# Optimization experiments

Measured on AMD Instinct MI355X. Metric: run time of the kernel, lower is better.

The kernel has to match this reference:

```python
import jax, jax.numpy as jnp
import numpy as np
import math
from functools import lru_cache

N_NODES = 30000
N_EDGES = 360000
IN_CH = 256
EDGE_DIM = 64

def parse_irreps(s):
    out = []
    for t in s.split('+'):
        t = t.strip()
        mul, lp = t.split('x')
        out.append((int(mul), int(lp[:-1]), 1 if lp[-1] == 'e' else -1))
    return out

IRR0 = parse_irreps('16x0e')
IRR1 = parse_irreps('16x0e + 2x1o + 2x2e')
IRR2 = parse_irreps('16x0e + 2x1o + 2x1e + 2x2e + 2x2o')
IRR3 = parse_irreps('2x0e + 2x0o + 2x1e + 2x1o + 2x2e + 2x2o + 2x3e + 2x3o')
SH_IRR = parse_irreps('1x0e + 1x1o + 1x2e')

def irreps_dim(irr):
    return sum(m * (2 * l + 1) for m, l, _ in irr)

def instructions(in1, in2, out):
    ins = []
    for i1, (m1, l1, p1) in enumerate(in1):
        for i2, (m2, l2, p2) in enumerate(in2):
            for io, (m3, l3, p3) in enumerate(out):
                if p1 * p2 == p3 and abs(l1 - l2) <= l3 <= l1 + l2:
                    ins.append((i1, i2, io, m1, m2, m3, l1, l2, l3))
    return ins

def weight_numel(in1, in2, out):
    return sum(t[3] * t[4] * t[5] for t in instructions(in1, in2, out))

def _su2_cg(j1, m1, j2, m2, j3, m3):
    if m3 != m1 + m2:
        return 0.0
    f = math.factorial
    vmin = max(-j1 + j2 + m3, -j1 + m1, 0)
    vmax = min(j2 + j3 + m1, j3 - j1 + j2, j3 + m3)
    if vmax < vmin:
        return 0.0
    c = math.sqrt((2 * j3 + 1) * f(j3 + j1 - j2) * f(j3 - j1 + j2) * f(j1 + j2 - j3) * f(j3 + m3) * f(j3 - m3) / (f(j1 + j2 + j3 + 1) * f(j1 - m1) * f(j1 + m1) * f(j2 - m2) * f(j2 + m2)))
    s = 0.0
    for v in range(vmin, vmax + 1):
        s += (-1.0) ** (v + j2 + m2) * f(j2 + j3 + m1 - v) * f(j1 - m1 + v) / (f(v) * f(j3 - j1 + j2 - v) * f(j3 + m3 - v) * f(v + j1 - j2 - m3))
    return c * s

def _q(l):
    q = np.zeros((2 * l + 1, 2 * l + 1), dtype=np.complex128)
    for m in range(-l, 0):
        q[l + m, l + abs(m)] = 2 ** -0.5
        q[l + m, l - abs(m)] = -1j * 2 ** -0.5
    q[l, l] = 1.0
    for m in range(1, l + 1):
        q[l + m, l + abs(m)] = (-1) ** m * 2 ** -0.5
        q[l + m, l - abs(m)] = 1j * (-1) ** m * 2 ** -0.5
    return (-1j) ** l * q

@lru_cache(maxsize=None)
def wigner_3j(l1, l2, l3):
    cg = np.zeros((2 * l1 + 1, 2 * l2 + 1, 2 * l3 + 1), dtype=np.complex128)
    for m1 in range(-l1, l1 + 1):
        for m2 in range(-l2, l2 + 1):
            for m3 in range(-l3, l3 + 1):
                cg[l1 + m1, l2 + m2, l3 + m3] = _su2_cg(l1, m1, l2, m2, l3, m3)
    c = np.einsum('ij,kl,nm,ikn->jlm', _q(l1), _q(l2), np.conj(_q(l3)), cg)
    cr, ci = np.real(c), np.imag(c)
    c = cr if np.linalg.norm(cr) >= np.linalg.norm(ci) else ci
    return jnp.asarray(c / np.linalg.norm(c), dtype=jnp.float32)

def slices(irr):
    offs, o = [], 0
    for m, l, _ in irr:
        offs.append(o)
        o += m * (2 * l + 1)
    return offs

def tensor_product(in1, in2, out, x1, x2, w):
    # e3nn FullyConnectedTensorProduct with external (per-edge) weights
    s1, s2, so = slices(in1), slices(in2), slices(out)
    ins = instructions(in1, in2, out)
    fan = {}
    for _, _, io, m1, m2, _, _, _, _ in ins:
        fan[io] = fan.get(io, 0) + m1 * m2
    e = x1.shape[0]
    res = jnp.zeros((e, irreps_dim(out)), x1.dtype)
    wo = 0
    for i1, i2, io, m1, m2, m3, l1, l2, l3 in ins:
        a = x1[:, s1[i1]:s1[i1] + m1 * (2 * l1 + 1)].reshape(e, m1, 2 * l1 + 1)
        b = x2[:, s2[i2]:s2[i2] + m2 * (2 * l2 + 1)].reshape(e, m2, 2 * l2 + 1)
        nw = m1 * m2 * m3
        ww = w[:, wo:wo + nw].reshape(e, m1, m2, m3)
        wo += nw
        c3 = wigner_3j(l1, l2, l3)
        alpha = math.sqrt((2 * l3 + 1) / fan[io])
        r = alpha * jnp.einsum('ijk,euvw,eui,evj->ewk', c3, ww, a, b)
        res = res.at[:, so[io]:so[io] + m3 * (2 * l3 + 1)].add(r.reshape(e, m3 * (2 * l3 + 1)))
    return res

def sph_harm(vec):
    # '1x0e + 1x1o + 1x2e', normalize=True, 'component' normalization
    n = jnp.sqrt(jnp.sum(vec * vec, axis=-1, keepdims=True))
    u = vec / jnp.maximum(n, 1e-12)
    x, y, z = u[..., 0], u[..., 1], u[..., 2]
    s3, s5, s15 = math.sqrt(3.0), math.sqrt(5.0), math.sqrt(15.0)
    return jnp.stack([jnp.ones_like(x), s3 * y, s3 * z, s3 * x, s15 * x * y, s15 * y * z, 0.5 * s5 * (3 * z * z - 1.0), s15 * x * z, 0.5 * s15 * (x * x - y * y)], axis=-1)

def conv_layer(in_irr, out_irr, node, edge_index, edge_feat, edge_sh, w1, b1, w2, b2, residual):
    src, dst = edge_index[0], edge_index[1]
    w = jax.nn.softplus(edge_feat @ w1 + b1) @ w2 + b2
    tp = tensor_product(in_irr, SH_IRR, out_irr, node[dst], edge_sh, w)
    n = node.shape[0]
    tot = jax.ops.segment_sum(tp, src, num_segments=n)
    cnt = jax.ops.segment_sum(jnp.ones((tp.shape[0],), tp.dtype), src, num_segments=n)
    out = tot / jnp.maximum(cnt, 1.0)[:, None]
    if residual:
        out = out + jnp.pad(node, ((0, 0), (0, out.shape[-1] - node.shape[-1])))
    return out

def _forward(node_feature, edge_vec, edge_feature, edge_index, lin_w, lin_b, f1w1, f1b1, f1w2, f1b2, f2w1, f2b1, f2w2, f2b2, f3w1, f3b1, f3w2, f3b2):
    edge_sh = sph_harm(edge_vec)
    h = node_feature @ lin_w + lin_b
    h = conv_layer(IRR0, IRR1, h, edge_index, edge_feature, edge_sh, f1w1, f1b1, f1w2, f1b2, True)
    h = conv_layer(IRR1, IRR2, h, edge_index, edge_feature, edge_sh, f2w1, f2b1, f2w2, f2b2, False)
    h = conv_layer(IRR2, IRR3, h, edge_index, edge_feature, edge_sh, f3w1, f3b1, f3w2, f3b2, False)
    return h

def setup_inputs() -> dict:
    key = jax.random.key(0)
    ks = jax.random.split(key, 20)
    def rn(k, shape, scale=1.0):
        return scale * jax.random.normal(k, shape, dtype=jnp.float32)
    inp = dict(
        node_feature=rn(ks[0], (N_NODES, IN_CH)),
        edge_vec=rn(ks[1], (N_EDGES, 3)),
        edge_feature=rn(ks[2], (N_EDGES, EDGE_DIM)),
        edge_index=jax.random.randint(ks[3], (2, N_EDGES), 0, N_NODES, dtype=jnp.int32),
        lin_w=rn(ks[4], (IN_CH, 16), IN_CH ** -0.5),
        lin_b=jnp.zeros((16,), jnp.float32),
    )
    wns = [weight_numel(IRR0, SH_IRR, IRR1), weight_numel(IRR1, SH_IRR, IRR2), weight_numel(IRR2, SH_IRR, IRR3)]
    for i, wn in enumerate(wns, 1):
        inp['fc%d_w1' % i] = rn(ks[4 + 4 * i], (EDGE_DIM, EDGE_DIM), EDGE_DIM ** -0.5)
        inp['fc%d_b1' % i] = jnp.zeros((EDGE_DIM,), jnp.float32)
        inp['fc%d_w2' % i] = rn(ks[5 + 4 * i], (EDGE_DIM, wn), EDGE_DIM ** -0.5)
        inp['fc%d_b2' % i] = jnp.zeros((wn,), jnp.float32)
    return inp

def reference(node_feature, edge_vec, edge_feature, edge_index, lin_w, lin_b, fc1_w1, fc1_b1, fc1_w2, fc1_b2, fc2_w1, fc2_b1, fc2_w2, fc2_b2, fc3_w1, fc3_b1, fc3_w2, fc3_b2):
    return _forward(node_feature, edge_vec, edge_feature, edge_index, lin_w, lin_b, fc1_w1, fc1_b1, fc1_w2, fc1_b2, fc2_w1, fc2_b1, fc2_w2, fc2_b2, fc3_w1, fc3_b1, fc3_w2, fc3_b2)
```

## Files before the change

### kernel.cpp

```cpp
#include <hip/hip_runtime.h>
#include <math.h>

#define EDGES 360000
#define NODES 30000
#define NB_SCAN 118
#define EPB 48

typedef _Float16 h2 __attribute__((ext_vector_type(2)));
typedef _Float16 h8 __attribute__((ext_vector_type(8)));

__device__ inline int imin(int a, int b){ return a < b ? a : b; }
__device__ inline int imax(int a, int b){ return a > b ? a : b; }

__device__ __forceinline__ float fdot2h(h2 a, h2 b, float c){
#if __has_builtin(__builtin_amdgcn_fdot2)
  return __builtin_amdgcn_fdot2(a, b, c, false);
#else
  return c + (float)a[0]*(float)b[0] + (float)a[1]*(float)b[1];
#endif
}

__device__ __forceinline__ float softplusf(float v){
  return fmaxf(v, 0.f) + log1pf(expf(-fabsf(v)));
}


struct cplx { double re, im; };
__device__ inline cplx cmul(cplx a, cplx b){ return { a.re*b.re - a.im*b.im, a.re*b.im + a.im*b.re }; }

__device__ __constant__ double FACT[9] = {1.0,1.0,2.0,6.0,24.0,120.0,720.0,5040.0,40320.0};

__device__ double su2_cg(int j1,int m1,int j2,int m2,int j3,int m3){
  if (m3 != m1 + m2) return 0.0;
  int vmin = imax(imax(-j1 + j2 + m3, -j1 + m1), 0);
  int vmax = imin(imin(j2 + j3 + m1, j3 - j1 + j2), j3 + m3);
  if (vmax < vmin) return 0.0;
  double c = sqrt((2.0*j3 + 1.0) * FACT[j3+j1-j2] * FACT[j3-j1+j2] * FACT[j1+j2-j3]
                  * FACT[j3+m3] * FACT[j3-m3]
                  / (FACT[j1+j2+j3+1] * FACT[j1-m1] * FACT[j1+m1] * FACT[j2-m2] * FACT[j2+m2]));
  double s = 0.0;
  for (int v = vmin; v <= vmax; ++v){
    double t = FACT[j2+j3+m1-v] * FACT[j1-m1+v]
             / (FACT[v] * FACT[j3-j1+j2-v] * FACT[j3+m3-v] * FACT[v+j1-j2-m3]);
    s += (((v + j2 + m2) & 1) ? -t : t);
  }
  return c * s;
}

__device__ cplx qval(int l, int r, int c){
  const double s = 0.7071067811865476;
  int m = r - l;
  cplx v = {0.0, 0.0};
  if (m < 0){
    if      (c == l - m) v = { s, 0.0 };
    else if (c == l + m) v = { 0.0, -s };
  } else if (m == 0){
    if (c == l) v = { 1.0, 0.0 };
  } else {
    double sg = (m & 1) ? -1.0 : 1.0;
    if      (c == l + m) v = { sg*s, 0.0 };
    else if (c == l - m) v = { 0.0, sg*s };
  }
  switch (l & 3){
    case 0: return v;
    case 1: return {  v.im, -v.re };
    case 2: return { -v.re, -v.im };
    default:return { -v.im,  v.re };
  }
}

struct Combo { int l1, l2, l3, off; };
__device__ __constant__ Combo COMBOS[18] = {
  {0,0,0,0},{0,1,1,1},{0,2,2,10},{1,0,1,35},{1,1,0,44},{1,1,1,53},{1,1,2,80},
  {1,2,1,125},{1,2,2,170},{1,2,3,245},{2,0,2,350},{2,1,1,375},{2,1,2,420},
  {2,1,3,495},{2,2,0,600},{2,2,1,625},{2,2,2,700},{2,2,3,825}
};

__global__ void init_cg_kernel(float* __restrict__ cg){
  __shared__ double sr[175], si[175];
  __shared__ double snorm[2];
  const Combo cb = COMBOS[blockIdx.x];
  const int d1 = 2*cb.l1+1, d2 = 2*cb.l2+1, d3 = 2*cb.l3+1;
  const int tot = d1*d2*d3;
  for (int idx = threadIdx.x; idx < tot; idx += blockDim.x){
    int j = idx/(d2*d3), rem = idx - j*(d2*d3);
    int l = rem/d3, m = rem - l*d3;
    double ar = 0.0, ai = 0.0;
    for (int i = 0; i < d1; ++i){
      cplx q1 = qval(cb.l1, i, j);
      if (q1.re == 0.0 && q1.im == 0.0) continue;
      for (int k = 0; k < d2; ++k){
        cplx q2 = qval(cb.l2, k, l);
        if (q2.re == 0.0 && q2.im == 0.0) continue;
        cplx q12 = cmul(q1, q2);
        for (int n = 0; n < d3; ++n){
          double g = su2_cg(cb.l1, i-cb.l1, cb.l2, k-cb.l2, cb.l3, n-cb.l3);
          if (g == 0.0) continue;
          cplx q3 = qval(cb.l3, n, m); q3.im = -q3.im;
          cplx t = cmul(q12, q3);
          ar += t.re * g; ai += t.im * g;
        }
      }
    }
    sr[idx] = ar; si[idx] = ai;
  }
  __syncthreads();
  if (threadIdx.x == 0){
    double nr = 0.0, ni = 0.0;
    for (int t = 0; t < tot; ++t){ nr += sr[t]*sr[t]; ni += si[t]*si[t]; }
    snorm[0] = nr; snorm[1] = ni;
  }
  __syncthreads();
  const bool useR = snorm[0] >= snorm[1];
  const double inv = 1.0 / sqrt(useR ? snorm[0] : snorm[1]);
  for (int idx = threadIdx.x; idx < tot; idx += blockDim.x)
    cg[cb.off + idx] = (float)((useR ? sr[idx] : si[idx]) * inv);
}


struct InsT { int l1,l2,l3,m1,m3,s1,s2,so,woff,cg; float alpha; };

struct L1 {
  static constexpr int NIN = 16, NOUT = 32, WN = 320, NI = 3, NWIN = 5, NU = 16, SW = 322;
  static constexpr InsT ins[NI] = {
    {0,0,0,16,16, 0,0, 0,   0,  0, 0.25f},
    {0,1,1,16, 2, 0,1,16, 256,  1, 0.4330127019f},
    {0,2,2,16, 2, 0,4,22, 288, 10, 0.5590169944f},
  };
  static constexpr int uT [NU] = {0,0,0,0,0,0,0,0, 1,1,1,1, 2,2,2,2};
  static constexpr int uCh[NU] = {0,1,2,3,4,5,6,7, 0,1,2,3, 0,1,2,3};
  static constexpr int uD0[NU] = {0,0,0,0,0,0,0,0, 0,0,0,0, 0,0,0,0};
  static constexpr int uND[NU] = {2,2,2,2,2,2,2,2, 4,4,4,4, 4,4,4,4};
  static constexpr int uPt[NU] = {0,0,0,0,0,0,0,0, 1,1,1,1, 2,2,2,2};
};
struct L2 {
  static constexpr int NIN = 32, NOUT = 48, WN = 424, NI = 15, NWIN = 7, NU = 30, SW = 426;
  static constexpr InsT ins[NI] = {
    {0,0,0,16,16, 0,0, 0,   0,  0, 0.2236067977f},
    {0,1,1,16, 2, 0,1,16, 256,  1, 0.3692744729f},
    {0,2,2,16, 2, 0,4,28, 288, 10, 0.4767312946f},
    {1,0,1, 2, 2,16,0,16, 320, 35, 0.3692744729f},
    {1,1,0, 2,16,16,1, 0, 324, 44, 0.2236067977f},
    {1,1,1, 2, 2,16,1,22, 356, 53, 0.8660254038f},
    {1,1,2, 2, 2,16,1,28, 360, 80, 0.4767312946f},
    {1,2,1, 2, 2,16,4,16, 364,125, 0.3692744729f},
    {1,2,2, 2, 2,16,4,38, 368,170, 1.1180339887f},
    {2,0,2, 2, 2,22,0,28, 372,350, 0.4767312946f},
    {2,1,1, 2, 2,22,1,16, 376,375, 0.3692744729f},
    {2,1,2, 2, 2,22,1,38, 380,420, 1.1180339887f},
    {2,2,0, 2,16,22,4, 0, 384,600, 0.2236067977f},
    {2,2,1, 2, 2,22,4,22, 416,625, 0.8660254038f},
    {2,2,2, 2, 2,22,4,28, 420,700, 0.4767312946f},
  };
  static constexpr int uT [NU] = {0,0,0,0,0,0,0,0, 1,1,1,1, 2,2,2,2, 3, 4,4, 5, 6,7,8, 9,10,11, 12,12, 13,14};
  static constexpr int uCh[NU] = {0,1,2,3,4,5,6,7, 0,1,2,3, 0,1,2,3, 0, 0,0, 0, 0,0,0, 0,0,0, 0,0, 0,0};
  static constexpr int uD0[NU] = {0,0,0,0,0,0,0,0, 0,0,0,0, 0,0,0,0, 0, 0,1, 0, 0,0,0, 0,0,0, 0,1, 0,0};
  static constexpr int uND[NU] = {2,2,2,2,2,2,2,2, 4,4,4,4, 4,4,4,4, 2, 1,1, 2, 2,2,2, 2,2,2, 1,1, 2,2};
  static constexpr int uPt[NU] = {0,0,0,0,0,0,0,0, 1,1,1,1, 2,2,2,2, 1, 0,0, 1, 2,1,3, 2,1,3, 0,0, 1,2};
};
struct L3 {
  static constexpr int NIN = 48, NOUT = 64, WN = 216, NI = 33, NWIN = 4, NU = 42, SW = 218;
  static constexpr InsT ins[NI] = {
    {0,0,0,16,2, 0,0, 0,   0,  0, 0.2236067977f},
    {0,1,1,16,2, 0,1,10,  32,  1, 0.3396831102f},
    {0,2,2,16,2, 0,4,16,  64, 10, 0.4385290097f},
    {1,0,1, 2,2,16,0,10,  96, 35, 0.3396831102f},
    {1,1,0, 2,2,16,1, 0, 100, 44, 0.2236067977f},
    {1,1,1, 2,2,16,1, 4, 104, 53, 0.5477225575f},
    {1,1,2, 2,2,16,1,16, 108, 80, 0.4385290097f},
    {1,2,1, 2,2,16,4,10, 112,125, 0.3396831102f},
    {1,2,2, 2,2,16,4,26, 116,170, 0.7071067812f},
    {1,2,3, 2,2,16,4,50, 120,245, 1.0801234497f},
    {1,0,1, 2,2,22,0, 4, 124, 35, 0.5477225575f},
    {1,1,0, 2,2,22,1, 2, 128, 44, 0.5f},
    {1,1,1, 2,2,22,1,10, 132, 53, 0.3396831102f},
    {1,1,2, 2,2,22,1,26, 136, 80, 0.7071067812f},
    {1,2,1, 2,2,22,4, 4, 140,125, 0.5477225575f},
    {1,2,2, 2,2,22,4,16, 144,170, 0.4385290097f},
    {1,2,3, 2,2,22,4,36, 148,245, 1.0801234497f},
    {2,0,2, 2,2,28,0,16, 152,350, 0.4385290097f},
    {2,1,1, 2,2,28,1,10, 156,375, 0.3396831102f},
    {2,1,2, 2,2,28,1,26, 160,420, 0.7071067812f},
    {2,1,3, 2,2,28,1,50, 164,495, 1.0801234497f},
    {2,2,0, 2,2,28,4, 0, 168,600, 0.2236067977f},
    {2,2,1, 2,2,28,4, 4, 172,625, 0.5477225575f},
    {2,2,2, 2,2,28,4,16, 176,700, 0.4385290097f},
    {2,2,3, 2,2,28,4,36, 180,825, 1.0801234497f},
    {2,0,2, 2,2,38,0,26, 184,350, 0.7071067812f},
    {2,1,1, 2,2,38,1, 4, 188,375, 0.5477225575f},
    {2,1,2, 2,2,38,1,16, 192,420, 0.4385290097f},
    {2,1,3, 2,2,38,1,36, 196,495, 1.0801234497f},
    {2,2,0, 2,2,38,4, 2, 200,600, 0.5f},
    {2,2,1, 2,2,38,4,10, 204,625, 0.3396831102f},
    {2,2,2, 2,2,38,4,26, 208,700, 0.7071067812f},
    {2,2,3, 2,2,38,4,50, 212,825, 1.0801234497f},
  };
  static constexpr int uT [NU] = {0,0,0,0, 1,1,1,1, 2,2,2,2,
    3,4,5,6,7,8,9,10,11,12,13,14,15,16,17,18,19,20,21,22,23,24,25,26,27,28,29,30,31,32};
  static constexpr int uCh[NU] = {0,1,2,3, 0,1,2,3, 0,1,2,3,
    0,0,0,0,0,0,0,0,0,0,0,0,0,0,0,0,0,0,0,0,0,0,0,0,0,0,0,0,0,0};
  static constexpr int uD0[NU] = {0,0,0,0, 0,0,0,0, 0,0,0,0,
    0,0,0,0,0,0,0,0,0,0,0,0,0,0,0,0,0,0,0,0,0,0,0,0,0,0,0,0,0,0};
  static constexpr int uND[NU] = {4,4,4,4, 4,4,4,4, 4,4,4,4,
    2,2,2,2,2,2,2,2,2,2,2,2,2,2,2,2,2,2,2,2,2,2,2,2,2,2,2,2,2,2};
  static constexpr int uPt[NU] = {0,0,0,0, 0,0,0,0, 1,1,1,1,
    0,0,0,1,0,1,3,0,0,0,1,0,1,2,1,0,1,3,0,0,1,2,1,0,1,2,0,0,1,3};
};


template<class LD>
constexpr int colsum(){
  int s = 0;
  for (int u = 0; u < LD::NU; ++u) s += LD::uND[u] * LD::ins[LD::uT[u]].m3;
  return s;
}
static_assert(colsum<L1>() == L1::WN, "L1 col coverage");
static_assert(colsum<L2>() == L2::WN, "L2 col coverage");
static_assert(colsum<L3>() == L3::WN, "L3 col coverage");

template<class LD, int PART>
constexpr int soLo(){
  int lo = 1 << 20;
  for (int u = 0; u < LD::NU; ++u){
    if (LD::uPt[u] != PART) continue;
    const InsT I = LD::ins[LD::uT[u]];
    if (I.so < lo) lo = I.so;
  }
  return lo;
}
template<class LD, int PART>
constexpr int soHi(){
  int hi = 0;
  for (int u = 0; u < LD::NU; ++u){
    if (LD::uPt[u] != PART) continue;
    const InsT I = LD::ins[LD::uT[u]];
    const int e = I.so + I.m3 * (2*I.l3 + 1);
    if (e > hi) hi = e;
  }
  return hi;
}
static_assert(soLo<L1,0>()==0 && soHi<L1,0>()==soLo<L1,1>() && soHi<L1,1>()==soLo<L1,2>()
           && soHi<L1,2>()==L1::NOUT && soHi<L1,3>()==0, "L1 parts");
static_assert(soLo<L2,0>()==0 && soHi<L2,0>()==soLo<L2,1>() && soHi<L2,1>()==soLo<L2,2>()
           && soHi<L2,2>()==soLo<L2,3>() && soHi<L2,3>()==L2::NOUT, "L2 parts");
static_assert(soLo<L3,0>()==0 && soHi<L3,0>()==soLo<L3,1>() && soHi<L3,1>()==soLo<L3,2>()
           && soHi<L3,2>()==soLo<L3,3>() && soHi<L3,3>()==L3::NOUT, "L3 parts");


template<class LD, int PART, int U, int NV>
__device__ __forceinline__ void tp_units(const char* wrow,
    const float* arow, const float* __restrict__ cgp,
    const float (&sh)[9], float (&outv)[NV])
{
  if constexpr (U < LD::NU) {
    if constexpr (LD::uPt[U] == PART) {
      constexpr InsT I = LD::ins[LD::uT[U]];
      constexpr int d1 = 2*I.l1+1, d2 = 2*I.l2+1, d3 = 2*I.l3+1;
      constexpr int UCH = (I.m3 == 16) ? 2 : (I.m1 == 16 ? 4 : 2);
      constexpr int base = I.woff + LD::uCh[U] * UCH * I.m3;
      constexpr int SOLO = soLo<LD,PART>();
      constexpr int D0 = LD::uD0[U];
      constexpr int ND = LD::uND[U];
      #pragma unroll
      for (int dd = 0; dd < ND; ++dd) {
        const int du = D0 + dd;
        const int u  = LD::uCh[U]*UCH + du;
        float ab[d3];
        #pragma unroll
        for (int k = 0; k < d3; ++k) ab[k] = 0.f;
        #pragma unroll
        for (int i = 0; i < d1; ++i) {
          const float ai = arow[I.s1 + u*d1 + i];
          #pragma unroll
          for (int j = 0; j < d2; ++j) {
            const float s = ai * sh[I.s2 + j];
            #pragma unroll
            for (int k = 0; k < d3; ++k)
              ab[k] = fmaf(cgp[I.cg + (i*d2 + j)*d3 + k], s, ab[k]);
          }
        }
        #pragma unroll
        for (int wo2 = 0; wo2 < I.m3/2; ++wo2) {
          const h2 wp = *(const h2*)(wrow + (base + du*I.m3 + 2*wo2)*2);
          const float wv0 = I.alpha * (float)wp[0];
          const float wv1 = I.alpha * (float)wp[1];
          #pragma unroll
          for (int k = 0; k < d3; ++k) {
            outv[I.so - SOLO + (2*wo2  )*d3 + k] =
              fmaf(wv0, ab[k], outv[I.so - SOLO + (2*wo2  )*d3 + k]);
            outv[I.so - SOLO + (2*wo2+1)*d3 + k] =
              fmaf(wv1, ab[k], outv[I.so - SOLO + (2*wo2+1)*d3 + k]);
          }
        }
      }
    }
    tp_units<LD, PART, U+1, NV>(wrow, arow, cgp, sh, outv);
  }
}

template<class LD, int PART>
__device__ __forceinline__ void run_part(const char* wrow, const float* arow,
    const float* __restrict__ cgp, const float (&sh)[9], float* dstp)
{
  constexpr int LO = soLo<LD,PART>();
  constexpr int HI = soHi<LD,PART>();
  if constexpr (HI > LO) {
    constexpr int NV = HI - LO;
    float outv[NV] = {};
    tp_units<LD, PART, 0, NV>(wrow, arow, cgp, sh, outv);
    #pragma unroll
    for (int o = 0; o < NV; ++o) dstp[LO + o] = outv[o];
  }
}

__global__ void pack_w2_kernel(const float* __restrict__ w2, float* __restrict__ dst,
                               int WN){
  const int hp = blockIdx.x;
  for (int c = threadIdx.x; c < WN; c += 256){
    h2 p;
    p[0] = (_Float16)w2[(size_t)(2*hp  )*WN + c];
    p[1] = (_Float16)w2[(size_t)(2*hp+1)*WN + c];
    *(h2*)((char*)dst + ((size_t)hp*WN + c)*4) = p;
  }
}


template<class LD>
__launch_bounds__(256, 3)
__global__ void conv_kernel(const float* __restrict__ node_h,
    const float* __restrict__ edge_vec, const float* __restrict__ edge_feat,
    const int* __restrict__ eidx,
    const float* __restrict__ w1, const float* __restrict__ b1,
    const float* __restrict__ w2h, const float* __restrict__ b2,
    const float* __restrict__ cgp, float* __restrict__ tp_out)
{
  constexpr int NIN = LD::NIN, NOUT = LD::NOUT, WN = LD::WN;
  constexpr int SB = LD::SW * 2;
  constexpr int WBYTES = EPB * SB;
  constexpr int OFF_HID = WBYTES;
  constexpr int OFF_AS  = WBYTES + 32*192;
  constexpr int SM_BYTES = OFF_AS + EPB*(NIN+1)*4;
  static_assert(SM_BYTES <= 65536, "static LDS limit");
  static_assert(32*192 <= WBYTES, "efsB must fit in W region");
  __shared__ __align__(16) char sm[SM_BYTES];
  char* Wls  = sm;
  char* efsB = sm;
  char* hidB = sm + OFF_HID;
  float* asB = (float*)(sm + OFF_AS);

  const int t = threadIdx.x;
  const int e0g = blockIdx.x * EPB;

  {
    const float4* efg = (const float4*)edge_feat + (size_t)e0g * 16;
    #pragma unroll
    for (int r = 0; r < 3; ++r) {
      const int f = r*256 + t;
      const int e = f >> 4, c0 = (f & 15) * 4;
      const float4 v = efg[f];
      h2 pa; pa[0] = (_Float16)v.x; pa[1] = (_Float16)v.y;
      h2 pb; pb[0] = (_Float16)v.z; pb[1] = (_Float16)v.w;
      *(h2*)(efsB + (c0>>1)*192 + e*4)     = pa;
      *(h2*)(efsB + ((c0>>1)+1)*192 + e*4) = pb;
    }
    for (int i = t; i < EPB*NIN; i += 256) {
      const int e = i / NIN, c = i - e*NIN;
      const int dst = eidx[EDGES + e0g + e];
      asB[e*(NIN+1) + c] = node_h[(size_t)dst*NIN + c];
    }
  }
  __syncthreads();

  {
    const int hg = t >> 3, eg2 = t & 7;
    const int h0 = hg*2, e0 = eg2*6;
    float acc[2][6];
    const float b10 = b1[h0], b11 = b1[h0+1];
    #pragma unroll
    for (int i = 0; i < 6; ++i) { acc[0][i] = b10; acc[1][i] = b11; }
    for (int cp = 0; cp < 32; ++cp) {
      h2 wp0, wp1;
      wp0[0] = (_Float16)w1[(size_t)(2*cp)*64 + h0];
      wp0[1] = (_Float16)w1[(size_t)(2*cp+1)*64 + h0];
      wp1[0] = (_Float16)w1[(size_t)(2*cp)*64 + h0+1];
      wp1[1] = (_Float16)w1[(size_t)(2*cp+1)*64 + h0+1];
      #pragma unroll
      for (int i = 0; i < 6; ++i) {
        const h2 e2 = *(const h2*)(efsB + cp*192 + (e0+i)*4);
        acc[0][i] = fdot2h(wp0, e2, acc[0][i]);
        acc[1][i] = fdot2h(wp1, e2, acc[1][i]);
      }
    }
    __syncthreads();
    #pragma unroll
    for (int i = 0; i < 6; ++i) {
      h2 p;
      p[0] = (_Float16)softplusf(acc[0][i]);
      p[1] = (_Float16)softplusf(acc[1][i]);
      *(h2*)(hidB + hg*192 + (e0+i)*4) = p;
    }
  }
  __syncthreads();

  {
    const int eg = t >> 4, cg = t & 15;
    const int e0 = eg*3;
    #pragma unroll
    for (int k = 0; k < LD::NWIN; ++k) {
      const int cb = k*64 + cg*4;
      if (cb < WN) {
        float acc[3][4];
        const float4 bv = *(const float4*)&b2[cb];
        const float bb[4] = {bv.x, bv.y, bv.z, bv.w};
        #pragma unroll
        for (int ei = 0; ei < 3; ++ei)
          #pragma unroll
          for (int ci = 0; ci < 4; ++ci) acc[ei][ci] = bb[ci];
        for (int hp = 0; hp < 32; ++hp) {
          const h8 wv = *(const h8*)((const char*)w2h + ((size_t)hp*WN + cb)*4);
          const h2 h0v = *(const h2*)(hidB + hp*192 + (e0+0)*4);
          const h2 h1v = *(const h2*)(hidB + hp*192 + (e0+1)*4);
          const h2 h2v = *(const h2*)(hidB + hp*192 + (e0+2)*4);
          #pragma unroll
          for (int ci = 0; ci < 4; ++ci) {
            const h2 wp = ((const h2*)&wv)[ci];
            acc[0][ci] = fdot2h(h0v, wp, acc[0][ci]);
            acc[1][ci] = fdot2h(h1v, wp, acc[1][ci]);
            acc[2][ci] = fdot2h(h2v, wp, acc[2][ci]);
          }
        }
        #pragma unroll
        for (int ei = 0; ei < 3; ++ei) {
          char* wp = Wls + (e0+ei)*SB + cb*2;
          h2 p0; p0[0] = (_Float16)acc[ei][0]; p0[1] = (_Float16)acc[ei][1];
          h2 p1; p1[0] = (_Float16)acc[ei][2]; p1[1] = (_Float16)acc[ei][3];
          *(h2*)(wp)     = p0;
          *(h2*)(wp + 4) = p1;
        }
      }
    }
  }
  __syncthreads();

  const int wave = t >> 6;
  const int lane = t & 63;
  if (lane < EPB) {
    const int le = lane;
    const int eme = e0g + le;
    float sh[9];
    {
      const float vx = edge_vec[(size_t)eme*3 + 0];
      const float vy = edge_vec[(size_t)eme*3 + 1];
      const float vz = edge_vec[(size_t)eme*3 + 2];
      const float nrm = sqrtf(vx*vx + vy*vy + vz*vz);
      const float invn = 1.0f / fmaxf(nrm, 1e-12f);
      const float x = vx*invn, y = vy*invn, z = vz*invn;
      sh[0] = 1.0f;
      sh[1] = 1.7320508076f * y;
      sh[2] = 1.7320508076f * z;
      sh[3] = 1.7320508076f * x;
      sh[4] = 3.8729833462f * x * y;
      sh[5] = 3.8729833462f * y * z;
      sh[6] = 1.1180339887f * (3.0f*z*z - 1.0f);
      sh[7] = 3.8729833462f * x * z;
      sh[8] = 1.9364916731f * (x*x - y*y);
    }
    const char* wrow  = Wls + le * SB;
    const float* arow = asB + le * (NIN + 1);
    float* dstp = tp_out + (size_t)eme * NOUT;
    switch (wave) {
      case 0:  run_part<LD,0>(wrow, arow, cgp, sh, dstp); break;
      case 1:  run_part<LD,1>(wrow, arow, cgp, sh, dstp); break;
      case 2:  run_part<LD,2>(wrow, arow, cgp, sh, dstp); break;
      default: run_part<LD,3>(wrow, arow, cgp, sh, dstp); break;
    }
  }
}


__global__ void cnt_kernel(const int* __restrict__ eidx, int* __restrict__ cnti){
  const int e = blockIdx.x * 256 + threadIdx.x;
  if (e < EDGES) atomicAdd(&cnti[eidx[e]], 1);
}

__global__ void scanA_kernel(const int* __restrict__ cnti, int* __restrict__ escan,
                             int* __restrict__ bsum){
  __shared__ int s[256];
  const int t = threadIdx.x, idx = blockIdx.x*256 + t;
  int v = (idx < NODES) ? cnti[idx] : 0;
  s[t] = v; __syncthreads();
  for (int off = 1; off < 256; off <<= 1){
    int x = (t >= off) ? s[t-off] : 0;
    __syncthreads();
    s[t] += x;
    __syncthreads();
  }
  if (idx < NODES) escan[idx] = s[t];
  if (t == 255) bsum[blockIdx.x] = s[255];
}

__global__ void scanB_kernel(const int* __restrict__ bsum, int* __restrict__ boff){
  __shared__ int s[128];
  const int t = threadIdx.x;
  int v = (t < NB_SCAN) ? bsum[t] : 0;
  s[t] = v; __syncthreads();
  for (int off = 1; off < 128; off <<= 1){
    int x = (t >= off) ? s[t-off] : 0;
    __syncthreads();
    s[t] += x;
    __syncthreads();
  }
  if (t < NB_SCAN) boff[t] = s[t] - v;
}

__global__ void scanC_kernel(const int* __restrict__ escan, const int* __restrict__ cnti,
                             const int* __restrict__ boff, int* __restrict__ eoff,
                             int* __restrict__ ecur){
  const int idx = blockIdx.x*256 + threadIdx.x;
  if (idx < NODES){
    const int v = escan[idx] - cnti[idx] + boff[blockIdx.x];
    eoff[idx] = v; ecur[idx] = v;
  }
  if (idx == 0) eoff[NODES] = EDGES;
}

__global__ void fill_eids_kernel(const int* __restrict__ eidx, int* __restrict__ ecur,
                                 int* __restrict__ eids){
  const int e = blockIdx.x * 256 + threadIdx.x;
  if (e < EDGES){
    const int p = atomicAdd(&ecur[eidx[e]], 1);
    eids[p] = e;
  }
}


template<int NOUT, bool RES>
__global__ void gather_kernel(const float* __restrict__ tp_out,
    const int* __restrict__ eoff, const int* __restrict__ eids,
    const float* __restrict__ h0, float* __restrict__ out)
{
  const int node = blockIdx.x * 4 + (threadIdx.x >> 6);
  const int lane = threadIdx.x & 63;
  if (node >= NODES) return;
  const int s = eoff[node], e_end = eoff[node+1];
  if (lane < NOUT) {
    float v = 0.f;
    for (int k = s; k < e_end; ++k) {
      const int e = eids[k];
      v += tp_out[(size_t)e*NOUT + lane];
    }
    v /= fmaxf((float)(e_end - s), 1.0f);
    if (RES && lane < 16) v += h0[node*16 + lane];
    out[(size_t)node*NOUT + lane] = v;
  }
}


__global__ void lin_kernel(const float* __restrict__ nf, const float* __restrict__ w,
                           const float* __restrict__ b, float* __restrict__ h0){
  const int idx = blockIdx.x * 256 + threadIdx.x;
  if (idx >= NODES * 16) return;
  const int n = idx >> 4, o = idx & 15;
  const float* __restrict__ row = nf + (size_t)n * 256;
  float acc = b[o];
  for (int c = 0; c < 256; ++c) acc = fmaf(row[c], w[c*16 + o], acc);
  h0[idx] = acc;
}


extern "C" void kernel_launch(void* const* d_in, const int* in_sizes, int n_in,
                              void* d_out, int out_size, void* d_ws, size_t ws_size,
                              hipStream_t stream) {
  (void)in_sizes; (void)n_in; (void)out_size; (void)ws_size;
  const float* node_feature = (const float*)d_in[0];
  const float* edge_vec     = (const float*)d_in[1];
  const float* edge_feature = (const float*)d_in[2];
  const int*   edge_index   = (const int*)d_in[3];
  const float* lin_w = (const float*)d_in[4];
  const float* lin_b = (const float*)d_in[5];
  const float* f1w1 = (const float*)d_in[6];
  const float* f1b1 = (const float*)d_in[7];
  const float* f1w2 = (const float*)d_in[8];
  const float* f1b2 = (const float*)d_in[9];
  const float* f2w1 = (const float*)d_in[10];
  const float* f2b1 = (const float*)d_in[11];
  const float* f2w2 = (const float*)d_in[12];
  const float* f2b2 = (const float*)d_in[13];
  const float* f3w1 = (const float*)d_in[14];
  const float* f3b1 = (const float*)d_in[15];
  const float* f3w2 = (const float*)d_in[16];
  const float* f3b2 = (const float*)d_in[17];

  float* ws   = (float*)d_ws;
  float* cg   = ws;
  int*   cnti = (int*)(ws + 1024);
  int*   escan= (int*)(ws + 32768);
  int*   bsum = (int*)(ws + 65536);
  int*   boff = (int*)(ws + 65792);
  int*   eoff = (int*)(ws + 66048);
  int*   ecur = (int*)(ws + 98304);
  int*   eids = (int*)(ws + 131072);
  float* w2h1 = ws + 491072;
  float* w2h2 = ws + 501312;
  float* w2h3 = ws + 514880;
  float* h0   = ws + 524288;
  float* h1   = ws + 1048576;
  float* h2p  = ws + 2097152;
  float* tpo  = ws + 3538944;
  float* outp = (float*)d_out;

  (void)hipMemsetAsync(cnti, 0, NODES * sizeof(int), stream);

  init_cg_kernel<<<18, 256, 0, stream>>>(cg);
  cnt_kernel<<<(EDGES + 255)/256, 256, 0, stream>>>(edge_index, cnti);
  scanA_kernel<<<NB_SCAN, 256, 0, stream>>>(cnti, escan, bsum);
  scanB_kernel<<<1, 128, 0, stream>>>(bsum, boff);
  scanC_kernel<<<NB_SCAN, 256, 0, stream>>>(escan, cnti, boff, eoff, ecur);
  fill_eids_kernel<<<(EDGES + 255)/256, 256, 0, stream>>>(edge_index, ecur, eids);
  lin_kernel<<<(NODES*16 + 255)/256, 256, 0, stream>>>(node_feature, lin_w, lin_b, h0);
  pack_w2_kernel<<<32, 256, 0, stream>>>(f1w2, w2h1, L1::WN);
  pack_w2_kernel<<<32, 256, 0, stream>>>(f2w2, w2h2, L2::WN);
  pack_w2_kernel<<<32, 256, 0, stream>>>(f3w2, w2h3, L3::WN);

  const int egrid = EDGES / EPB;
  const int ggrid = (NODES + 3) / 4;

  conv_kernel<L1><<<egrid, 256, 0, stream>>>(h0, edge_vec, edge_feature, edge_index,
                                             f1w1, f1b1, w2h1, f1b2, cg, tpo);
  gather_kernel<32, true><<<ggrid, 256, 0, stream>>>(tpo, eoff, eids, h0, h1);

  conv_kernel<L2><<<egrid, 256, 0, stream>>>(h1, edge_vec, edge_feature, edge_index,
                                             f2w1, f2b1, w2h2, f2b2, cg, tpo);
  gather_kernel<48, false><<<ggrid, 256, 0, stream>>>(tpo, eoff, eids, h0, h2p);

  conv_kernel<L3><<<egrid, 256, 0, stream>>>(h2p, edge_vec, edge_feature, edge_index,
                                             f3w1, f3b1, w2h3, f3b2, cg, tpo);
  gather_kernel<64, false><<<ggrid, 256, 0, stream>>>(tpo, eoff, eids, h0, outp);
}
```

Before: 1.563 ms.

## Raise edges per block to 60 and store gathered node features as fp16 in LDS

Each block now processes 60 edges instead of 48. The per-thread tiles in the two MLP stages grow accordingly (8 and 4 edges per thread, with tail guards), and the LDS strides change from 192 to 256. The gathered source-node features are now held in LDS as fp16 rather than fp32, which halves that buffer and lets the larger tile fit. The occupancy hint of 3 in launch_bounds is dropped. The aim is fewer blocks and better reuse of the FC2 weight reads, at the cost of less precision on node inputs and possibly lower occupancy.

```diff
diff --git a/kernel.cpp b/kernel.cpp
--- a/kernel.cpp
+++ b/kernel.cpp
@@ -4,7 +4,7 @@
 #define EDGES 360000
 #define NODES 30000
 #define NB_SCAN 118
-#define EPB 48
+#define EPB 60
 
 typedef _Float16 h2 __attribute__((ext_vector_type(2)));
 typedef _Float16 h8 __attribute__((ext_vector_type(8)));
@@ -249,7 +249,7 @@
 
 template<class LD, int PART, int U, int NV>
 __device__ __forceinline__ void tp_units(const char* wrow,
-    const float* arow, const float* __restrict__ cgp,
+    const char* arowB, const float* __restrict__ cgp,
     const float (&sh)[9], float (&outv)[NV])
 {
   if constexpr (U < LD::NU) {
@@ -270,7 +270,7 @@
         for (int k = 0; k < d3; ++k) ab[k] = 0.f;
         #pragma unroll
         for (int i = 0; i < d1; ++i) {
-          const float ai = arow[I.s1 + u*d1 + i];
+          const float ai = (float)*(const _Float16*)(arowB + (I.s1 + u*d1 + i)*2);
           #pragma unroll
           for (int j = 0; j < d2; ++j) {
             const float s = ai * sh[I.s2 + j];
@@ -294,12 +294,12 @@
         }
       }
     }
-    tp_units<LD, PART, U+1, NV>(wrow, arow, cgp, sh, outv);
+    tp_units<LD, PART, U+1, NV>(wrow, arowB, cgp, sh, outv);
   }
 }
 
 template<class LD, int PART>
-__device__ __forceinline__ void run_part(const char* wrow, const float* arow,
+__device__ __forceinline__ void run_part(const char* wrow, const char* arowB,
     const float* __restrict__ cgp, const float (&sh)[9], float* dstp)
 {
   constexpr int LO = soLo<LD,PART>();
@@ -307,7 +307,7 @@
   if constexpr (HI > LO) {
     constexpr int NV = HI - LO;
     float outv[NV] = {};
-    tp_units<LD, PART, 0, NV>(wrow, arow, cgp, sh, outv);
+    tp_units<LD, PART, 0, NV>(wrow, arowB, cgp, sh, outv);
     #pragma unroll
     for (int o = 0; o < NV; ++o) dstp[LO + o] = outv[o];
   }
@@ -326,7 +326,7 @@
 
 
 template<class LD>
-__launch_bounds__(256, 3)
+__launch_bounds__(256)
 __global__ void conv_kernel(const float* __restrict__ node_h,
     const float* __restrict__ edge_vec, const float* __restrict__ edge_feat,
     const int* __restrict__ eidx,
@@ -336,17 +336,18 @@
 {
   constexpr int NIN = LD::NIN, NOUT = LD::NOUT, WN = LD::WN;
   constexpr int SB = LD::SW * 2;
+  constexpr int SA = NIN + 1;
   constexpr int WBYTES = EPB * SB;
   constexpr int OFF_HID = WBYTES;
-  constexpr int OFF_AS  = WBYTES + 32*192;
-  constexpr int SM_BYTES = OFF_AS + EPB*(NIN+1)*4;
+  constexpr int OFF_AS  = WBYTES + 32*256;
+  constexpr int SM_BYTES = OFF_AS + EPB*SA*2;
   static_assert(SM_BYTES <= 65536, "static LDS limit");
-  static_assert(32*192 <= WBYTES, "efsB must fit in W region");
+  static_assert(32*256 <= WBYTES, "efsB must fit in W region");
   __shared__ __align__(16) char sm[SM_BYTES];
   char* Wls  = sm;
   char* efsB = sm;
   char* hidB = sm + OFF_HID;
-  float* asB = (float*)(sm + OFF_AS);
+  char* asB  = sm + OFF_AS;
 
   const int t = threadIdx.x;
   const int e0g = blockIdx.x * EPB;
@@ -354,30 +355,33 @@
   {
     const float4* efg = (const float4*)edge_feat + (size_t)e0g * 16;
     #pragma unroll
-    for (int r = 0; r < 3; ++r) {
+    for (int r = 0; r < 4; ++r) {
       const int f = r*256 + t;
-      const int e = f >> 4, c0 = (f & 15) * 4;
-      const float4 v = efg[f];
-      h2 pa; pa[0] = (_Float16)v.x; pa[1] = (_Float16)v.y;
-      h2 pb; pb[0] = (_Float16)v.z; pb[1] = (_Float16)v.w;
-      *(h2*)(efsB + (c0>>1)*192 + e*4)     = pa;
-      *(h2*)(efsB + ((c0>>1)+1)*192 + e*4) = pb;
+      if (f < EPB*16) {
+        const int e = f >> 4, c0 = (f & 15) * 4;
+        const float4 v = efg[f];
+        h2 pa; pa[0] = (_Float16)v.x; pa[1] = (_Float16)v.y;
+        h2 pb; pb[0] = (_Float16)v.z; pb[1] = (_Float16)v.w;
+        *(h2*)(efsB + (c0>>1)*256 + e*4)     = pa;
+        *(h2*)(efsB + ((c0>>1)+1)*256 + e*4) = pb;
+      }
     }
     for (int i = t; i < EPB*NIN; i += 256) {
       const int e = i / NIN, c = i - e*NIN;
       const int dst = eidx[EDGES + e0g + e];
-      asB[e*(NIN+1) + c] = node_h[(size_t)dst*NIN + c];
+      *(_Float16*)(asB + (e*SA + c)*2) = (_Float16)node_h[(size_t)dst*NIN + c];
     }
   }
   __syncthreads();
 
   {
     const int hg = t >> 3, eg2 = t & 7;
-    const int h0 = hg*2, e0 = eg2*6;
-    float acc[2][6];
+    const int h0 = hg*2, e0 = eg2*8;
+    const int ne = (EPB - e0 < 8) ? (EPB - e0) : 8;
+    float acc[2][8];
     const float b10 = b1[h0], b11 = b1[h0+1];
     #pragma unroll
-    for (int i = 0; i < 6; ++i) { acc[0][i] = b10; acc[1][i] = b11; }
+    for (int i = 0; i < 8; ++i) { acc[0][i] = b10; acc[1][i] = b11; }
     for (int cp = 0; cp < 32; ++cp) {
       h2 wp0, wp1;
       wp0[0] = (_Float16)w1[(size_t)(2*cp)*64 + h0];
@@ -385,57 +389,63 @@
       wp1[0] = (_Float16)w1[(size_t)(2*cp)*64 + h0+1];
       wp1[1] = (_Float16)w1[(size_t)(2*cp+1)*64 + h0+1];
       #pragma unroll
-      for (int i = 0; i < 6; ++i) {
-        const h2 e2 = *(const h2*)(efsB + cp*192 + (e0+i)*4);
-        acc[0][i] = fdot2h(wp0, e2, acc[0][i]);
-        acc[1][i] = fdot2h(wp1, e2, acc[1][i]);
+      for (int i = 0; i < 8; ++i) {
+        if (i < ne) {
+          const h2 e2 = *(const h2*)(efsB + cp*256 + (e0+i)*4);
+          acc[0][i] = fdot2h(wp0, e2, acc[0][i]);
+          acc[1][i] = fdot2h(wp1, e2, acc[1][i]);
+        }
       }
     }
     __syncthreads();
     #pragma unroll
-    for (int i = 0; i < 6; ++i) {
-      h2 p;
-      p[0] = (_Float16)softplusf(acc[0][i]);
-      p[1] = (_Float16)softplusf(acc[1][i]);
-      *(h2*)(hidB + hg*192 + (e0+i)*4) = p;
+    for (int i = 0; i < 8; ++i) {
+      if (i < ne) {
+        h2 p;
+        p[0] = (_Float16)softplusf(acc[0][i]);
+        p[1] = (_Float16)softplusf(acc[1][i]);
+        *(h2*)(hidB + hg*256 + (e0+i)*4) = p;
+      }
     }
   }
   __syncthreads();
 
   {
     const int eg = t >> 4, cg = t & 15;
-    const int e0 = eg*3;
+    const int e0 = eg*4;
+    const int ne = (EPB - e0 < 4) ? imax(EPB - e0, 0) : 4;
     #pragma unroll
     for (int k = 0; k < LD::NWIN; ++k) {
       const int cb = k*64 + cg*4;
-      if (cb < WN) {
-        float acc[3][4];
+      if (cb < WN && ne > 0) {
+        float acc[4][4];
         const float4 bv = *(const float4*)&b2[cb];
         const float bb[4] = {bv.x, bv.y, bv.z, bv.w};
         #pragma unroll
-        for (int ei = 0; ei < 3; ++ei)
+        for (int ei = 0; ei < 4; ++ei)
           #pragma unroll
           for (int ci = 0; ci < 4; ++ci) acc[ei][ci] = bb[ci];
         for (int hp = 0; hp < 32; ++hp) {
           const h8 wv = *(const h8*)((const char*)w2h + ((size_t)hp*WN + cb)*4);
-          const h2 h0v = *(const h2*)(hidB + hp*192 + (e0+0)*4);
-          const h2 h1v = *(const h2*)(hidB + hp*192 + (e0+1)*4);
-          const h2 h2v = *(const h2*)(hidB + hp*192 + (e0+2)*4);
           #pragma unroll
-          for (int ci = 0; ci < 4; ++ci) {
-            const h2 wp = ((const h2*)&wv)[ci];
-            acc[0][ci] = fdot2h(h0v, wp, acc[0][ci]);
-            acc[1][ci] = fdot2h(h1v, wp, acc[1][ci]);
-            acc[2][ci] = fdot2h(h2v, wp, acc[2][ci]);
+          for (int ei = 0; ei < 4; ++ei) {
+            if (ei < ne) {
+              const h2 hv = *(const h2*)(hidB + hp*256 + (e0+ei)*4);
+              #pragma unroll
+              for (int ci = 0; ci < 4; ++ci)
+                acc[ei][ci] = fdot2h(hv, ((const h2*)&wv)[ci], acc[ei][ci]);
+            }
           }
         }
         #pragma unroll
-        for (int ei = 0; ei < 3; ++ei) {
-          char* wp = Wls + (e0+ei)*SB + cb*2;
-          h2 p0; p0[0] = (_Float16)acc[ei][0]; p0[1] = (_Float16)acc[ei][1];
-          h2 p1; p1[0] = (_Float16)acc[ei][2]; p1[1] = (_Float16)acc[ei][3];
-          *(h2*)(wp)     = p0;
-          *(h2*)(wp + 4) = p1;
+        for (int ei = 0; ei < 4; ++ei) {
+          if (ei < ne) {
+            char* wp = Wls + (e0+ei)*SB + cb*2;
+            h2 p0; p0[0] = (_Float16)acc[ei][0]; p0[1] = (_Float16)acc[ei][1];
+            h2 p1; p1[0] = (_Float16)acc[ei][2]; p1[1] = (_Float16)acc[ei][3];
+            *(h2*)(wp)     = p0;
+            *(h2*)(wp + 4) = p1;
+          }
         }
       }
     }
@@ -466,13 +476,13 @@
       sh[8] = 1.9364916731f * (x*x - y*y);
     }
     const char* wrow  = Wls + le * SB;
-    const float* arow = asB + le * (NIN + 1);
+    const char* arowB = asB + le * SA * 2;
     float* dstp = tp_out + (size_t)eme * NOUT;
     switch (wave) {
-      case 0:  run_part<LD,0>(wrow, arow, cgp, sh, dstp); break;
-      case 1:  run_part<LD,1>(wrow, arow, cgp, sh, dstp); break;
-      case 2:  run_part<LD,2>(wrow, arow, cgp, sh, dstp); break;
-      default: run_part<LD,3>(wrow, arow, cgp, sh, dstp); break;
+      case 0:  run_part<LD,0>(wrow, arowB, cgp, sh, dstp); break;
+      case 1:  run_part<LD,1>(wrow, arowB, cgp, sh, dstp); break;
+      case 2:  run_part<LD,2>(wrow, arowB, cgp, sh, dstp); break;
+      default: run_part<LD,3>(wrow, arowB, cgp, sh, dstp); break;
     }
   }
 }
```

New measurement: 2.464 ms. 57.7% more time.
